# Performance work log

Measured on AMD Instinct MI355X. Metric: run time of the kernel, lower is better.

The kernel has to match this reference:

```python
import jax, jax.numpy as jnp
import numpy as np


def _chamfer(pred, tgt):
    # pred: [B,N,3], tgt: [B,M,3]
    # Euclidean pairwise distances (same math as torch.cdist, p=2)
    p2 = jnp.sum(pred * pred, axis=-1)              # [B,N]
    t2 = jnp.sum(tgt * tgt, axis=-1)                # [B,M]
    cross = jnp.einsum('bnd,bmd->bnm', pred, tgt)   # [B,N,M]
    sq = p2[:, :, None] + t2[:, None, :] - 2.0 * cross
    dist = jnp.sqrt(jnp.maximum(sq, 0.0))           # [B,N,M]
    min_p2t = jnp.min(dist, axis=2)                 # [B,N]
    min_t2p = jnp.min(dist, axis=1)                 # [B,M]
    return jnp.mean(min_p2t) + jnp.mean(min_t2p)


def setup_inputs() -> dict:
    key = jax.random.key(0)
    k1, k2 = jax.random.split(key)
    B, N, M, D = 8, 4096, 4096, 3
    predicted_points = jax.random.normal(k1, (B, N, D), dtype=jnp.float32)
    target_points = jax.random.normal(k2, (B, M, D), dtype=jnp.float32)
    return {"predicted_points": predicted_points, "target_points": target_points}


def reference(predicted_points, target_points):
    return _chamfer(predicted_points, target_points)
```

## Files before the change

### kernel.cpp

```cpp
#include <hip/hip_runtime.h>
#include <math.h>

#define B_SZ 8
#define N_SZ 4096
#define M_SZ 4096
#define NQ (B_SZ * N_SZ)
#define TOT (2 * NQ)

#define THREADS 256
#define QPT 8
#define SLOTS (QPT / 2)
#define QPB (THREADS * QPT)
#define ITILES (N_SZ / QPB)
#define JTILE 256
#define NJT (M_SZ / JTILE)

#define NBLK2 (TOT / 256)

typedef float f32x2 __attribute__((ext_vector_type(2)));


__global__ __launch_bounds__(THREADS)
void chamfer_partial_kernel(const float* __restrict__ pred,
                            const float* __restrict__ tgt,
                            float* __restrict__ part)
{
    const int b   = blockIdx.y;
    const int dir = blockIdx.z;

    const float* Q;
    const float* Db;
    int qoff;
    if (dir == 0) { Q = pred + (size_t)b * N_SZ * 3; Db = tgt  + (size_t)b * M_SZ * 3; qoff = b * N_SZ; }
    else          { Q = tgt  + (size_t)b * M_SZ * 3; Db = pred + (size_t)b * N_SZ * 3; qoff = NQ + b * M_SZ; }

    const int itile = blockIdx.x >> 4;
    const int g     = blockIdx.x & (NJT - 1);

    __shared__ float4 sp[JTILE];
    {
        const float* s = Db + (size_t)(g * JTILE + threadIdx.x) * 3;
        float x = s[0], y = s[1], z = s[2];
        sp[threadIdx.x] = make_float4(x, y, z, 0.5f * (x * x + y * y + z * z));
    }
    __syncthreads();

    f32x2 qxn[SLOTS], qyn[SLOTS], qzn[SLOTS], q2h[SLOTS], mn[SLOTS];
    const int qbase = itile * QPB + threadIdx.x;
#pragma unroll
    for (int s = 0; s < SLOTS; ++s) {
        const int i0 = qbase + (2 * s) * THREADS;
        const int i1 = qbase + (2 * s + 1) * THREADS;
        float x0 = Q[i0 * 3 + 0], y0 = Q[i0 * 3 + 1], z0 = Q[i0 * 3 + 2];
        float x1 = Q[i1 * 3 + 0], y1 = Q[i1 * 3 + 1], z1 = Q[i1 * 3 + 2];
        qxn[s] = { -x0, -x1 };
        qyn[s] = { -y0, -y1 };
        qzn[s] = { -z0, -z1 };
        q2h[s] = { 0.5f * (x0 * x0 + y0 * y0 + z0 * z0),
                   0.5f * (x1 * x1 + y1 * y1 + z1 * z1) };
        mn[s]  = { 3.0e38f, 3.0e38f };
    }

#pragma unroll 8
    for (int j = 0; j < JTILE; ++j) {
        float4 t = sp[j];
        f32x2 tx = { t.x, t.x };
        f32x2 ty = { t.y, t.y };
        f32x2 tz = { t.z, t.z };
        f32x2 th = { t.w, t.w };
#pragma unroll
        for (int s = 0; s < SLOTS; ++s) {
            f32x2 sc = th + qxn[s] * tx;
            sc += qyn[s] * ty;
            sc += qzn[s] * tz;
            mn[s].x = fminf(mn[s].x, sc.x);
            mn[s].y = fminf(mn[s].y, sc.y);
        }
    }

    float* pg = part + (size_t)g * TOT + qoff;
#pragma unroll
    for (int s = 0; s < SLOTS; ++s) {
        f32x2 v = mn[s] + q2h[s];
        pg[qbase + (2 * s) * THREADS]     = v.x;
        pg[qbase + (2 * s + 1) * THREADS] = v.y;
    }
}

__global__ __launch_bounds__(256)
void chamfer_combine_kernel(const float* __restrict__ part,
                            float* __restrict__ bsum)
{
    const int q = blockIdx.x * 256 + threadIdx.x;
    float m = 3.0e38f;
#pragma unroll
    for (int g = 0; g < NJT; ++g) m = fminf(m, part[(size_t)g * TOT + q]);
    float d = sqrtf(2.0f * fmaxf(m, 0.0f));
#pragma unroll
    for (int off = 32; off > 0; off >>= 1) d += __shfl_down(d, off);
    __shared__ float r[4];
    if ((threadIdx.x & 63) == 0) r[threadIdx.x >> 6] = d;
    __syncthreads();
    if (threadIdx.x == 0) bsum[blockIdx.x] = r[0] + r[1] + r[2] + r[3];
}

__global__ __launch_bounds__(64)
void chamfer_final_kernel(const float* __restrict__ bsum,
                          float* __restrict__ out)
{
    float s = 0.0f;
#pragma unroll
    for (int i = 0; i < NBLK2 / 64; ++i) s += bsum[threadIdx.x + i * 64];
#pragma unroll
    for (int off = 32; off > 0; off >>= 1) s += __shfl_down(s, off);
    if (threadIdx.x == 0) out[0] = s * (1.0f / (float)NQ);
}

extern "C" void kernel_launch(void* const* d_in, const int* in_sizes, int n_in,
                              void* d_out, int out_size, void* d_ws, size_t ws_size,
                              hipStream_t stream) {
    const float* pred = (const float*)d_in[0];
    const float* tgt  = (const float*)d_in[1];
    float* out = (float*)d_out;

    float* part = (float*)d_ws;
    float* bsum = part + (size_t)NJT * TOT;

    dim3 grid1(ITILES * NJT, B_SZ, 2);
    chamfer_partial_kernel<<<grid1, THREADS, 0, stream>>>(pred, tgt, part);
    chamfer_combine_kernel<<<NBLK2, 256, 0, stream>>>(part, bsum);
    chamfer_final_kernel<<<1, 64, 0, stream>>>(bsum, out);
}
```

Before: 78.62 us.

## Pack target pairs into packed-math lanes, fold final reduction into atomics

Measured after the change: 83.77 us. 6.5% more time.

```diff
diff --git a/kernel.cpp b/kernel.cpp
--- a/kernel.cpp
+++ b/kernel.cpp
@@ -9,24 +9,27 @@
 
 #define THREADS 256
 #define QPT 8
-#define SLOTS (QPT / 2)
 #define QPB (THREADS * QPT)
 #define ITILES (N_SZ / QPB)
 #define JTILE 256
 #define NJT (M_SZ / JTILE)
+#define JPAIRS (JTILE / 2)
 
 #define NBLK2 (TOT / 256)
 
 typedef float f32x2 __attribute__((ext_vector_type(2)));
 
-
 __global__ __launch_bounds__(THREADS)
 void chamfer_partial_kernel(const float* __restrict__ pred,
                             const float* __restrict__ tgt,
-                            float* __restrict__ part)
+                            float* __restrict__ part,
+                            float* __restrict__ out)
 {
     const int b   = blockIdx.y;
     const int dir = blockIdx.z;
+
+    if (blockIdx.x == 0 && b == 0 && dir == 0 && threadIdx.x == 0)
+        out[0] = 0.0f;
 
     const float* Q;
     const float* Db;
@@ -37,59 +40,63 @@
     const int itile = blockIdx.x >> 4;
     const int g     = blockIdx.x & (NJT - 1);
 
-    __shared__ float4 sp[JTILE];
+    __shared__ float4 spA[JPAIRS];
+    __shared__ float4 spB[JPAIRS];
     {
-        const float* s = Db + (size_t)(g * JTILE + threadIdx.x) * 3;
+        const int k = threadIdx.x;
+        const float* s = Db + (size_t)(g * JTILE + k) * 3;
         float x = s[0], y = s[1], z = s[2];
-        sp[threadIdx.x] = make_float4(x, y, z, 0.5f * (x * x + y * y + z * z));
+        float h = 0.5f * (x * x + y * y + z * z);
+        float* A  = (float*)&spA[k >> 1];
+        float* Bv = (float*)&spB[k >> 1];
+        const int hsel = k & 1;
+        A[hsel]      = x;
+        A[2 + hsel]  = y;
+        Bv[hsel]     = z;
+        Bv[2 + hsel] = h;
+    }
+
+    f32x2 qxn[QPT], qyn[QPT], qzn[QPT];
+    float q2h[QPT], mn[QPT];
+    const int qbase = itile * QPB + threadIdx.x;
+#pragma unroll
+    for (int i = 0; i < QPT; ++i) {
+        const int qi = qbase + i * THREADS;
+        float x = Q[qi * 3 + 0], y = Q[qi * 3 + 1], z = Q[qi * 3 + 2];
+        qxn[i] = { -x, -x };
+        qyn[i] = { -y, -y };
+        qzn[i] = { -z, -z };
+        q2h[i] = 0.5f * (x * x + y * y + z * z);
+        mn[i]  = 3.0e38f;
     }
     __syncthreads();
 
-    f32x2 qxn[SLOTS], qyn[SLOTS], qzn[SLOTS], q2h[SLOTS], mn[SLOTS];
-    const int qbase = itile * QPB + threadIdx.x;
+#pragma unroll 4
+    for (int j = 0; j < JPAIRS; ++j) {
+        float4 A  = spA[j];
+        float4 Bv = spB[j];
+        f32x2 tx = { A.x,  A.y  };
+        f32x2 ty = { A.z,  A.w  };
+        f32x2 tz = { Bv.x, Bv.y };
+        f32x2 th = { Bv.z, Bv.w };
 #pragma unroll
-    for (int s = 0; s < SLOTS; ++s) {
-        const int i0 = qbase + (2 * s) * THREADS;
-        const int i1 = qbase + (2 * s + 1) * THREADS;
-        float x0 = Q[i0 * 3 + 0], y0 = Q[i0 * 3 + 1], z0 = Q[i0 * 3 + 2];
-        float x1 = Q[i1 * 3 + 0], y1 = Q[i1 * 3 + 1], z1 = Q[i1 * 3 + 2];
-        qxn[s] = { -x0, -x1 };
-        qyn[s] = { -y0, -y1 };
-        qzn[s] = { -z0, -z1 };
-        q2h[s] = { 0.5f * (x0 * x0 + y0 * y0 + z0 * z0),
-                   0.5f * (x1 * x1 + y1 * y1 + z1 * z1) };
-        mn[s]  = { 3.0e38f, 3.0e38f };
-    }
-
-#pragma unroll 8
-    for (int j = 0; j < JTILE; ++j) {
-        float4 t = sp[j];
-        f32x2 tx = { t.x, t.x };
-        f32x2 ty = { t.y, t.y };
-        f32x2 tz = { t.z, t.z };
-        f32x2 th = { t.w, t.w };
-#pragma unroll
-        for (int s = 0; s < SLOTS; ++s) {
-            f32x2 sc = th + qxn[s] * tx;
-            sc += qyn[s] * ty;
-            sc += qzn[s] * tz;
-            mn[s].x = fminf(mn[s].x, sc.x);
-            mn[s].y = fminf(mn[s].y, sc.y);
+        for (int i = 0; i < QPT; ++i) {
+            f32x2 sc = th + qxn[i] * tx;
+            sc += qyn[i] * ty;
+            sc += qzn[i] * tz;
+            mn[i] = fminf(mn[i], fminf(sc.x, sc.y));
         }
     }
 
     float* pg = part + (size_t)g * TOT + qoff;
 #pragma unroll
-    for (int s = 0; s < SLOTS; ++s) {
-        f32x2 v = mn[s] + q2h[s];
-        pg[qbase + (2 * s) * THREADS]     = v.x;
-        pg[qbase + (2 * s + 1) * THREADS] = v.y;
-    }
+    for (int i = 0; i < QPT; ++i)
+        pg[qbase + i * THREADS] = mn[i] + q2h[i];
 }
 
 __global__ __launch_bounds__(256)
 void chamfer_combine_kernel(const float* __restrict__ part,
-                            float* __restrict__ bsum)
+                            float* __restrict__ out)
 {
     const int q = blockIdx.x * 256 + threadIdx.x;
     float m = 3.0e38f;
@@ -101,19 +108,8 @@
     __shared__ float r[4];
     if ((threadIdx.x & 63) == 0) r[threadIdx.x >> 6] = d;
     __syncthreads();
-    if (threadIdx.x == 0) bsum[blockIdx.x] = r[0] + r[1] + r[2] + r[3];
-}
-
-__global__ __launch_bounds__(64)
-void chamfer_final_kernel(const float* __restrict__ bsum,
-                          float* __restrict__ out)
-{
-    float s = 0.0f;
-#pragma unroll
-    for (int i = 0; i < NBLK2 / 64; ++i) s += bsum[threadIdx.x + i * 64];
-#pragma unroll
-    for (int off = 32; off > 0; off >>= 1) s += __shfl_down(s, off);
-    if (threadIdx.x == 0) out[0] = s * (1.0f / (float)NQ);
+    if (threadIdx.x == 0)
+        atomicAdd(out, (r[0] + r[1] + r[2] + r[3]) * (1.0f / (float)NQ));
 }
 
 extern "C" void kernel_launch(void* const* d_in, const int* in_sizes, int n_in,
@@ -124,10 +120,8 @@
     float* out = (float*)d_out;
 
     float* part = (float*)d_ws;
-    float* bsum = part + (size_t)NJT * TOT;
 
     dim3 grid1(ITILES * NJT, B_SZ, 2);
-    chamfer_partial_kernel<<<grid1, THREADS, 0, stream>>>(pred, tgt, part);
-    chamfer_combine_kernel<<<NBLK2, 256, 0, stream>>>(part, bsum);
-    chamfer_final_kernel<<<1, 64, 0, stream>>>(bsum, out);
+    chamfer_partial_kernel<<<grid1, THREADS, 0, stream>>>(pred, tgt, part, out);
+    chamfer_combine_kernel<<<NBLK2, 256, 0, stream>>>(part, out);
 }
```
